# Kernel tuning notes

Measured on AMD Instinct MI355X. Metric: run time of the kernel, lower is better.

## Reference

```python
import jax, jax.numpy as jnp
import numpy as np

B, VD, SD, CD, H, HEADS = 16384, 2048, 1024, 512, 256, 4
DH = H // HEADS
EPS = 1e-5


def layer_norm(x, g, b):
    m = jnp.mean(x, axis=-1, keepdims=True)
    v = jnp.var(x, axis=-1, keepdims=True)
    return (x - m) * jax.lax.rsqrt(v + EPS) * g + b


def setup_inputs() -> dict:
    key = jax.random.key(0)
    ks = jax.random.split(key, 16)
    sc = 0.02
    inp = {
        'fv': jax.random.normal(ks[0], (B, VD), jnp.float32),
        'fs': jax.random.normal(ks[1], (B, SD), jnp.float32),
        'fc': jax.random.normal(ks[2], (B, CD), jnp.float32),
        # projection linears + layernorms
        'Wv': jax.random.normal(ks[3], (H, VD), jnp.float32) * sc,
        'bv': jnp.zeros((H,), jnp.float32),
        'gv': jnp.ones((H,), jnp.float32), 'bev': jnp.zeros((H,), jnp.float32),
        'Ws': jax.random.normal(ks[4], (H, SD), jnp.float32) * sc,
        'bs': jnp.zeros((H,), jnp.float32),
        'gs': jnp.ones((H,), jnp.float32), 'bes': jnp.zeros((H,), jnp.float32),
        'Wc': jax.random.normal(ks[5], (H, CD), jnp.float32) * sc,
        'bc': jnp.zeros((H,), jnp.float32),
        'gc_': jnp.ones((H,), jnp.float32), 'bec': jnp.zeros((H,), jnp.float32),
        # MultiheadAttention packed in-proj and out-proj
        'in_w': jax.random.normal(ks[6], (3 * H, H), jnp.float32) * sc,
        'in_b': jnp.zeros((3 * H,), jnp.float32),
        'out_w': jax.random.normal(ks[7], (H, H), jnp.float32) * sc,
        'out_b': jnp.zeros((H,), jnp.float32),
        # post-attention layernorm
        'gn': jnp.ones((H,), jnp.float32), 'gb': jnp.zeros((H,), jnp.float32),
        # gating MLP: Linear(3H,64) -> GELU -> Linear(64,3) -> softmax
        'g1w': jax.random.normal(ks[8], (64, 3 * H), jnp.float32) * sc,
        'g1b': jnp.zeros((64,), jnp.float32),
        'g2w': jax.random.normal(ks[9], (3, 64), jnp.float32) * sc,
        'g2b': jnp.zeros((3,), jnp.float32),
    }
    return inp


def reference(fv, fs, fc, Wv, bv, gv, bev, Ws, bs, gs, bes, Wc, bc, gc_, bec,
              in_w, in_b, out_w, out_b, gn, gb, g1w, g1b, g2w, g2b):
    v = layer_norm(fv @ Wv.T + bv, gv, bev)   # [B,H]
    s = layer_norm(fs @ Ws.T + bs, gs, bes)
    c = layer_norm(fc @ Wc.T + bc, gc_, bec)
    stack = jnp.stack([v, s, c], axis=1)      # [B,3,H]

    # self-attention over seq=3 (eval mode: dropout off)
    qkv = stack @ in_w.T + in_b               # [B,3,3H]
    q, k, vv = jnp.split(qkv, 3, axis=-1)
    def heads(x):  # [B,3,H] -> [B,HEADS,3,DH]
        return x.reshape(B, 3, HEADS, DH).transpose(0, 2, 1, 3)
    q, k, vv = heads(q), heads(k), heads(vv)
    scores = jnp.einsum('bhqd,bhkd->bhqk', q, k) / jnp.sqrt(jnp.float32(DH))
    attn = jax.nn.softmax(scores, axis=-1)
    ctx = jnp.einsum('bhqk,bhkd->bhqd', attn, vv)
    ctx = ctx.transpose(0, 2, 1, 3).reshape(B, 3, H)
    attended = ctx @ out_w.T + out_b          # [B,3,H]

    attended = layer_norm(attended + stack, gn, gb)
    av, as_, ac = attended[:, 0], attended[:, 1], attended[:, 2]

    h1 = jax.nn.gelu(jnp.concatenate([av, as_, ac], axis=-1) @ g1w.T + g1b, approximate=False)
    gates = jax.nn.softmax(h1 @ g2w.T + g2b, axis=-1)  # [B,3]

    fused = gates[:, 0:1] * av + gates[:, 1:2] * as_ + gates[:, 2:3] * ac
    return (fused, gates)
```

## Files before the change

kernel.cpp:

```cpp
#include <hip/hip_runtime.h>
#include <math.h>


typedef unsigned short u16;
typedef __bf16 bf16x8 __attribute__((ext_vector_type(8)));
typedef float fx4 __attribute__((ext_vector_type(4)));

#define MFMA_BF16(A_, B_, C_) __builtin_amdgcn_mfma_f32_16x16x32_bf16((A_), (B_), (C_), 0, 0, 0)

__device__ __forceinline__ float bf2f(u16 s) {
    union { float f; unsigned u; } c; c.u = ((unsigned)s) << 16; return c.f;
}
__device__ __forceinline__ u16 f2bf(float f) {
    union { float f; unsigned u; } c; c.f = f;
    return (u16)((c.u + 0x7fffu + ((c.u >> 16) & 1u)) >> 16);
}
__device__ __forceinline__ float bfpair_dot(unsigned a, unsigned b) {
    union { unsigned u; float f; } al, ah, bl, bh;
    al.u = a << 16; ah.u = a & 0xffff0000u;
    bl.u = b << 16; bh.u = b & 0xffff0000u;
    return al.f * bl.f + ah.f * bh.f;
}
__device__ __forceinline__ void gld16(void* l, const void* g) {
    __builtin_amdgcn_global_load_lds((const __attribute__((address_space(1))) void*)g,
                                     (__attribute__((address_space(3))) void*)l, 16, 0, 0);
}

__global__ __launch_bounds__(256) void cvt_w(const float* Wv, const float* Ws, const float* Wc,
                                             const float* inw, const float* outw, const float* g1w,
                                             u16* dst) {
    int idx = blockIdx.x * 256 + threadIdx.x;
    const float* src; int rel;
    if      (idx <  524288) { src = Wv;   rel = idx; }
    else if (idx <  786432) { src = Ws;   rel = idx -  524288; }
    else if (idx <  917504) { src = Wc;   rel = idx -  786432; }
    else if (idx < 1114112) { src = inw;  rel = idx -  917504; }
    else if (idx < 1179648) { src = outw; rel = idx - 1114112; }
    else                    { src = g1w;  rel = idx - 1179648; }
    dst[idx] = f2bf(src[rel]);
}

__global__ __launch_bounds__(256, 3) void gemm_ln(
    const float* fv, const float* fs, const float* fc,
    const u16* wWv, const u16* wWs, const u16* wWc,
    const float* bv, const float* gv, const float* bev,
    const float* bs, const float* gs, const float* bes,
    const float* bc, const float* gc_, const float* bec,
    u16* stack) {
    __shared__ alignas(16) char smem[45568];
    u16* sC = (u16*)smem;
    float* redS = (float*)(smem + 43008);
    float* redQ = (float*)(smem + 44032);
    float* mvS  = (float*)(smem + 45056);

    int bid = blockIdx.x;
    int slot, mblk;
    if (bid < 256)      { slot = 0; mblk = bid; }
    else if (bid < 512) { slot = 1; mblk = bid - 256; }
    else                { slot = 2; mblk = bid - 512; }

    const float* A; const u16* W; const float* bias; const float* gg; const float* be; int K;
    if (slot == 0)      { A = fv; W = wWv; bias = bv; gg = gv;  be = bev; K = 2048; }
    else if (slot == 1) { A = fs; W = wWs; bias = bs; gg = gs;  be = bes; K = 1024; }
    else                { A = fc; W = wWc; bias = bc; gg = gc_; be = bec; K = 512;  }

    int t = threadIdx.x, wv = t >> 6, ln = t & 63, q = ln >> 4, l15 = ln & 15;
    int m0 = mblk * 64;

    fx4 zero = {0.f, 0.f, 0.f, 0.f};
    fx4 acc[4][4];
    #pragma unroll
    for (int mi = 0; mi < 4; ++mi)
        #pragma unroll
        for (int ni = 0; ni < 4; ++ni) acc[mi][ni] = zero;

    int rowA = t >> 2, ca = t & 3;
    const float* aBase = A + (size_t)(m0 + rowA) * K + ca * 8;
    int sAwOff = rowA * 40 + ca * 8;

    int bN[4], bKc[4], bDst[4];
    #pragma unroll
    for (int i = 0; i < 4; ++i) {
        int d = wv * 256 + i * 64 + ln;
        bN[i] = d >> 2;
        bKc[i] = (d & 3) ^ ((bN[i] >> 1) & 3);
        bDst[i] = (wv * 256 + i * 64) * 16;
    }

    int niter = K >> 5;

    {
        float4 f0 = *(const float4*)(aBase);
        float4 f1 = *(const float4*)(aBase + 4);
        #pragma unroll
        for (int i = 0; i < 4; ++i)
            gld16(smem + 10240 + bDst[i], W + (size_t)bN[i] * K + bKc[i] * 8);
        union { u16 us[8]; uint4 v; } pk;
        pk.us[0] = f2bf(f0.x); pk.us[1] = f2bf(f0.y); pk.us[2] = f2bf(f0.z); pk.us[3] = f2bf(f0.w);
        pk.us[4] = f2bf(f1.x); pk.us[5] = f2bf(f1.y); pk.us[6] = f2bf(f1.z); pk.us[7] = f2bf(f1.w);
        *(uint4*)((u16*)smem + sAwOff) = pk.v;
    }
    __syncthreads();

    for (int kt = 0; kt < niter; ++kt) {
        int cur = kt & 1, nxt_b = (kt + 1) & 1;
        u16* sAc = (u16*)(smem + cur * 5120);
        u16* sBc = (u16*)(smem + 10240 + cur * 16384);
        int has_next = (kt + 1) < niter;

        float4 nf0, nf1;
        if (has_next) {
            nf0 = *(const float4*)(aBase + (kt + 1) * 32);
            nf1 = *(const float4*)(aBase + (kt + 1) * 32 + 4);
            char* sBn = smem + 10240 + nxt_b * 16384;
            #pragma unroll
            for (int i = 0; i < 4; ++i)
                gld16(sBn + bDst[i], W + (size_t)bN[i] * K + (kt + 1) * 32 + bKc[i] * 8);
        }

        bf16x8 af[4], bfr[4];
        #pragma unroll
        for (int mi = 0; mi < 4; ++mi)
            af[mi] = *(const bf16x8*)(sAc + (mi * 16 + l15) * 40 + q * 8);
        #pragma unroll
        for (int ni = 0; ni < 4; ++ni) {
            int n = wv * 64 + ni * 16 + l15;
            int ch = n * 4 + (q ^ ((n >> 1) & 3));
            bfr[ni] = *(const bf16x8*)(sBc + ch * 8);
        }
        #pragma unroll
        for (int mi = 0; mi < 4; ++mi)
            #pragma unroll
            for (int ni = 0; ni < 4; ++ni)
                acc[mi][ni] = MFMA_BF16(af[mi], bfr[ni], acc[mi][ni]);

        if (has_next) {
            union { u16 us[8]; uint4 v; } pk;
            pk.us[0] = f2bf(nf0.x); pk.us[1] = f2bf(nf0.y); pk.us[2] = f2bf(nf0.z); pk.us[3] = f2bf(nf0.w);
            pk.us[4] = f2bf(nf1.x); pk.us[5] = f2bf(nf1.y); pk.us[6] = f2bf(nf1.z); pk.us[7] = f2bf(nf1.w);
            *(uint4*)((u16*)(smem + nxt_b * 5120) + sAwOff) = pk.v;
        }
        __syncthreads();
    }

    float biasv[4], gvv[4], bevv[4];
    #pragma unroll
    for (int ni = 0; ni < 4; ++ni) {
        int col = wv * 64 + ni * 16 + l15;
        biasv[ni] = bias[col]; gvv[ni] = gg[col]; bevv[ni] = be[col];
    }
    #pragma unroll
    for (int mi = 0; mi < 4; ++mi)
        #pragma unroll
        for (int ni = 0; ni < 4; ++ni)
            #pragma unroll
            for (int r = 0; r < 4; ++r) acc[mi][ni][r] += biasv[ni];
    #pragma unroll
    for (int mi = 0; mi < 4; ++mi) {
        #pragma unroll
        for (int r = 0; r < 4; ++r) {
            float s = 0.f, qq = 0.f;
            #pragma unroll
            for (int ni = 0; ni < 4; ++ni) { float x = acc[mi][ni][r]; s += x; qq += x * x; }
            #pragma unroll
            for (int m = 1; m < 16; m <<= 1) { s += __shfl_xor(s, m, 64); qq += __shfl_xor(qq, m, 64); }
            if (l15 == 0) { int rho = mi * 16 + q * 4 + r; redS[rho * 4 + wv] = s; redQ[rho * 4 + wv] = qq; }
        }
    }
    __syncthreads();
    if (t < 64) {
        float s = redS[t * 4] + redS[t * 4 + 1] + redS[t * 4 + 2] + redS[t * 4 + 3];
        float qq = redQ[t * 4] + redQ[t * 4 + 1] + redQ[t * 4 + 2] + redQ[t * 4 + 3];
        float mean = s * (1.f / 256.f);
        float var = qq * (1.f / 256.f) - mean * mean;
        mvS[t * 2] = mean; mvS[t * 2 + 1] = rsqrtf(var + 1e-5f);
    }
    __syncthreads();
    #pragma unroll
    for (int mi = 0; mi < 4; ++mi) {
        #pragma unroll
        for (int r = 0; r < 4; ++r) {
            int rho = mi * 16 + q * 4 + r;
            float mean = mvS[rho * 2], rstd = mvS[rho * 2 + 1];
            #pragma unroll
            for (int ni = 0; ni < 4; ++ni) {
                int col = wv * 64 + ni * 16 + l15;
                float x = (acc[mi][ni][r] - mean) * rstd * gvv[ni] + bevv[ni];
                sC[rho * 256 + col] = f2bf(x);
            }
        }
    }
    __syncthreads();
    u16* outp = stack + (size_t)m0 * 768 + slot * 256;
    #pragma unroll
    for (int it = 0; it < 8; ++it) {
        int idx = t + it * 256;
        int row = idx >> 5, c = idx & 31;
        uint4 v = *(const uint4*)(sC + row * 256 + c * 8);
        *(uint4*)(outp + (size_t)row * 768 + c * 8) = v;
    }
}

__global__ __launch_bounds__(256) void gemm_qkv(const u16* stack, const u16* W, const float* in_b,
                                                u16* qkv) {
    __shared__ alignas(16) char smem[32768];
    u16* sC = (u16*)smem;

    int t = threadIdx.x, wv = t >> 6, ln = t & 63, q = ln >> 4, l15 = ln & 15;
    int n0 = blockIdx.x * 128, m0 = blockIdx.y * 128;
    int wr = wv >> 1, wc = wv & 1;

    fx4 zero = {0.f, 0.f, 0.f, 0.f};
    fx4 acc[4][4];
    #pragma unroll
    for (int mi = 0; mi < 4; ++mi)
        #pragma unroll
        for (int ni = 0; ni < 4; ++ni) acc[mi][ni] = zero;

    int sR[2], sKc[2], sDst[2];
    #pragma unroll
    for (int i = 0; i < 2; ++i) {
        int d = wv * 128 + i * 64 + ln;
        sR[i] = d >> 2;
        sKc[i] = (d & 3) ^ ((sR[i] >> 1) & 3);
        sDst[i] = (wv * 128 + i * 64) * 16;
    }

    #pragma unroll
    for (int i = 0; i < 2; ++i) {
        gld16(smem + sDst[i],         stack + (size_t)(m0 + sR[i]) * 256 + sKc[i] * 8);
        gld16(smem + 16384 + sDst[i], W     + (size_t)(n0 + sR[i]) * 256 + sKc[i] * 8);
    }
    __syncthreads();

    for (int kt = 0; kt < 8; ++kt) {
        int cur = kt & 1, nxt_b = (kt + 1) & 1;
        if (kt < 7) {
            #pragma unroll
            for (int i = 0; i < 2; ++i) {
                gld16(smem + nxt_b * 8192 + sDst[i],
                      stack + (size_t)(m0 + sR[i]) * 256 + (kt + 1) * 32 + sKc[i] * 8);
                gld16(smem + 16384 + nxt_b * 8192 + sDst[i],
                      W + (size_t)(n0 + sR[i]) * 256 + (kt + 1) * 32 + sKc[i] * 8);
            }
        }
        u16* sAc = (u16*)(smem + cur * 8192);
        u16* sBc = (u16*)(smem + 16384 + cur * 8192);
        bf16x8 af[4], bfr[4];
        #pragma unroll
        for (int mi = 0; mi < 4; ++mi) {
            int r = wr * 64 + mi * 16 + l15;
            int ch = r * 4 + (q ^ ((r >> 1) & 3));
            af[mi] = *(const bf16x8*)(sAc + ch * 8);
        }
        #pragma unroll
        for (int ni = 0; ni < 4; ++ni) {
            int n = wc * 64 + ni * 16 + l15;
            int ch = n * 4 + (q ^ ((n >> 1) & 3));
            bfr[ni] = *(const bf16x8*)(sBc + ch * 8);
        }
        #pragma unroll
        for (int mi = 0; mi < 4; ++mi)
            #pragma unroll
            for (int ni = 0; ni < 4; ++ni)
                acc[mi][ni] = MFMA_BF16(af[mi], bfr[ni], acc[mi][ni]);
        __syncthreads();
    }
    float biasv[4];
    #pragma unroll
    for (int ni = 0; ni < 4; ++ni) biasv[ni] = in_b[n0 + wc * 64 + ni * 16 + l15];
    #pragma unroll
    for (int mi = 0; mi < 4; ++mi)
        #pragma unroll
        for (int ni = 0; ni < 4; ++ni)
            #pragma unroll
            for (int r = 0; r < 4; ++r) {
                int rl = wr * 64 + mi * 16 + q * 4 + r;
                int cl = wc * 64 + ni * 16 + l15;
                sC[rl * 128 + cl] = f2bf(acc[mi][ni][r] + biasv[ni]);
            }
    __syncthreads();
    #pragma unroll
    for (int it = 0; it < 8; ++it) {
        int idx = t + it * 256;
        int row = idx >> 4, c = idx & 15;
        uint4 v = *(const uint4*)(sC + row * 128 + c * 8);
        *(uint4*)(qkv + (size_t)(m0 + row) * 768 + n0 + c * 8) = v;
    }
}

__global__ __launch_bounds__(256) void attn_k(const u16* qkv, u16* ctx) {
    __shared__ alignas(16) char smem[38016];
    u16* qs = (u16*)smem;
    float* sS = (float*)(smem + 36864);

    int t = threadIdx.x, wv = t >> 6, ln = t & 63;
    size_t base = (size_t)blockIdx.x * 8 * 2304;
    #pragma unroll
    for (int i = 0; i < 9; ++i) {
        int d = wv * 576 + i * 64;
        gld16((char*)smem + (size_t)d * 16, qkv + base + (size_t)(d + ln) * 8);
    }
    __syncthreads();
    #pragma unroll
    for (int it = 0; it < 2; ++it) {
        int idx = t + it * 256;
        if (idx < 288) {
            int b = idx / 36, rem = idx % 36, h = rem / 9, pp = rem % 9, i = pp / 3, j = pp % 3;
            const u16* qp = qs + b * 2304 + i * 768 + h * 64;
            const u16* kp = qs + b * 2304 + j * 768 + 256 + h * 64;
            float acc = 0.f;
            #pragma unroll
            for (int c = 0; c < 8; ++c) {
                uint4 qa = *(const uint4*)(qp + c * 8);
                uint4 ka = *(const uint4*)(kp + c * 8);
                acc += bfpair_dot(qa.x, ka.x) + bfpair_dot(qa.y, ka.y) +
                       bfpair_dot(qa.z, ka.z) + bfpair_dot(qa.w, ka.w);
            }
            sS[idx] = acc * 0.125f;
        }
    }
    __syncthreads();
    if (t < 96) {
        int b3 = t * 3;
        float s0 = sS[b3], s1 = sS[b3 + 1], s2 = sS[b3 + 2];
        float m = fmaxf(s0, fmaxf(s1, s2));
        float e0 = __expf(s0 - m), e1 = __expf(s1 - m), e2 = __expf(s2 - m);
        float inv = 1.f / (e0 + e1 + e2);
        sS[b3] = e0 * inv; sS[b3 + 1] = e1 * inv; sS[b3 + 2] = e2 * inv;
    }
    __syncthreads();
    #pragma unroll
    for (int it = 0; it < 3; ++it) {
        int idx = t + it * 256;
        int b = idx / 96, rem = idx % 96, i = rem / 32, c = rem & 31, h = c >> 3;
        int pbase = b * 36 + h * 9 + i * 3;
        float o[8];
        #pragma unroll
        for (int e = 0; e < 8; ++e) o[e] = 0.f;
        #pragma unroll
        for (int j = 0; j < 3; ++j) {
            float p = sS[pbase + j];
            uint4 va = *(const uint4*)(qs + b * 2304 + j * 768 + 512 + c * 8);
            unsigned uu[4] = {va.x, va.y, va.z, va.w};
            #pragma unroll
            for (int pr = 0; pr < 4; ++pr) {
                union { unsigned u; float f; } lo, hi;
                lo.u = uu[pr] << 16; hi.u = uu[pr] & 0xffff0000u;
                o[2 * pr]     += p * lo.f;
                o[2 * pr + 1] += p * hi.f;
            }
        }
        union { u16 us[8]; uint4 v; } pk;
        #pragma unroll
        for (int e = 0; e < 8; ++e) pk.us[e] = f2bf(o[e]);
        *(uint4*)(ctx + (size_t)(blockIdx.x * 8 + b) * 768 + i * 256 + c * 8) = pk.v;
    }
}

__global__ __launch_bounds__(256) void outproj_k(
    const u16* ctx, const u16* W, const float* out_b, const u16* stack,
    const float* gn, const float* gb, const u16* g1w, const float* g1b,
    const float* g2w, const float* g2b, float* outF, float* outG) {
    __shared__ alignas(16) char smem[40960];
    u16* r1 = (u16*)smem;
    u16* sB = (u16*)(smem + 24576);
    float* redS = (float*)(smem + 24576);
    float* redQ = redS + 192;
    float* mvS = redQ + 192;
    float* h1S = (float*)(smem + 26624);
    float* lgS = (float*)(smem + 30720);
    float* gateS = lgS + 48;

    int t = threadIdx.x, wv = t >> 6, ln = t & 63, q = ln >> 4, l15 = ln & 15;
    int gr0 = blockIdx.x * 48, b0 = blockIdx.x * 16;

    #pragma unroll
    for (int i = 0; i < 6; ++i) {
        int d = wv * 384 + i * 64 + ln;
        int row = d >> 5, p = d & 31;
        int kc = p ^ (row & 7);
        gld16((char*)r1 + (wv * 384 + i * 64) * 16, ctx + (size_t)(gr0 + row) * 256 + kc * 8);
    }
    __syncthreads();

    fx4 zero = {0.f, 0.f, 0.f, 0.f};
    fx4 acc[3][4];
    #pragma unroll
    for (int mi = 0; mi < 3; ++mi)
        #pragma unroll
        for (int ni = 0; ni < 4; ++ni) acc[mi][ni] = zero;

    for (int kt = 0; kt < 8; ++kt) {
        #pragma unroll
        for (int i = 0; i < 4; ++i) {
            int d = wv * 256 + i * 64 + ln;
            int n = d >> 2, p = d & 3;
            int kc = p ^ ((n >> 1) & 3);
            gld16((char*)sB + (wv * 256 + i * 64) * 16, W + (size_t)n * 256 + kt * 32 + kc * 8);
        }
        __syncthreads();
        bf16x8 af[3], bfr[4];
        #pragma unroll
        for (int mi = 0; mi < 3; ++mi) {
            int row = mi * 16 + l15;
            int ch = row * 32 + ((kt * 4 + q) ^ (row & 7));
            af[mi] = *(const bf16x8*)(r1 + ch * 8);
        }
        #pragma unroll
        for (int ni = 0; ni < 4; ++ni) {
            int n = wv * 64 + ni * 16 + l15;
            int ch = n * 4 + (q ^ ((n >> 1) & 3));
            bfr[ni] = *(const bf16x8*)(sB + ch * 8);
        }
        #pragma unroll
        for (int mi = 0; mi < 3; ++mi)
            #pragma unroll
            for (int ni = 0; ni < 4; ++ni)
                acc[mi][ni] = MFMA_BF16(af[mi], bfr[ni], acc[mi][ni]);
        __syncthreads();
    }

    #pragma unroll
    for (int i = 0; i < 6; ++i) {
        int d = wv * 384 + i * 64 + ln;
        gld16((char*)r1 + (wv * 384 + i * 64) * 16, stack + (size_t)gr0 * 256 + (size_t)d * 8);
    }
    __syncthreads();

    float obv[4], gnv[4], gbv[4];
    #pragma unroll
    for (int ni = 0; ni < 4; ++ni) {
        int col = wv * 64 + ni * 16 + l15;
        obv[ni] = out_b[col]; gnv[ni] = gn[col]; gbv[ni] = gb[col];
    }
    #pragma unroll
    for (int mi = 0; mi < 3; ++mi)
        #pragma unroll
        for (int ni = 0; ni < 4; ++ni)
            #pragma unroll
            for (int r = 0; r < 4; ++r) {
                int rho = mi * 16 + q * 4 + r;
                int col = wv * 64 + ni * 16 + l15;
                acc[mi][ni][r] += obv[ni] + bf2f(r1[rho * 256 + col]);
            }
    #pragma unroll
    for (int mi = 0; mi < 3; ++mi) {
        #pragma unroll
        for (int r = 0; r < 4; ++r) {
            float s = 0.f, qq = 0.f;
            #pragma unroll
            for (int ni = 0; ni < 4; ++ni) { float x = acc[mi][ni][r]; s += x; qq += x * x; }
            #pragma unroll
            for (int m = 1; m < 16; m <<= 1) { s += __shfl_xor(s, m, 64); qq += __shfl_xor(qq, m, 64); }
            if (l15 == 0) { int rho = mi * 16 + q * 4 + r; redS[rho * 4 + wv] = s; redQ[rho * 4 + wv] = qq; }
        }
    }
    __syncthreads();
    if (t < 48) {
        float s = redS[t * 4] + redS[t * 4 + 1] + redS[t * 4 + 2] + redS[t * 4 + 3];
        float qq = redQ[t * 4] + redQ[t * 4 + 1] + redQ[t * 4 + 2] + redQ[t * 4 + 3];
        float mean = s * (1.f / 256.f);
        float var = qq * (1.f / 256.f) - mean * mean;
        mvS[t * 2] = mean; mvS[t * 2 + 1] = rsqrtf(var + 1e-5f);
    }
    __syncthreads();
    #pragma unroll
    for (int mi = 0; mi < 3; ++mi) {
        #pragma unroll
        for (int r = 0; r < 4; ++r) {
            int rho = mi * 16 + q * 4 + r;
            float mean = mvS[rho * 2], rstd = mvS[rho * 2 + 1];
            int bl = rho / 3, sl = rho - bl * 3;
            #pragma unroll
            for (int ni = 0; ni < 4; ++ni) {
                int col = wv * 64 + ni * 16 + l15;
                float x = (acc[mi][ni][r] - mean) * rstd * gnv[ni] + gbv[ni];
                int k = sl * 256 + col;
                int kidx = k >> 3, wn = k & 7;
                r1[(bl * 96 + (kidx ^ (bl & 7))) * 8 + wn] = f2bf(x);
            }
        }
    }
    __syncthreads();
    fx4 ag = zero;
    for (int kt = 0; kt < 24; ++kt) {
        int bl = l15;
        int kidx = kt * 4 + q;
        bf16x8 afr = *(const bf16x8*)(r1 + (bl * 96 + (kidx ^ (bl & 7))) * 8);
        int n = wv * 16 + l15;
        bf16x8 bfr2 = *(const bf16x8*)(g1w + (size_t)n * 768 + kt * 32 + q * 8);
        ag = MFMA_BF16(afr, bfr2, ag);
    }
    #pragma unroll
    for (int r = 0; r < 4; ++r) {
        int bl = q * 4 + r, n = wv * 16 + l15;
        float x = ag[r] + g1b[n];
        h1S[bl * 64 + n] = 0.5f * x * (1.f + erff(x * 0.70710678118f));
    }
    __syncthreads();
    if (t < 48) {
        int bl = t / 3, s = t - bl * 3;
        float a = g2b[s];
        #pragma unroll
        for (int k = 0; k < 64; ++k) a += h1S[bl * 64 + k] * g2w[s * 64 + k];
        lgS[t] = a;
    }
    __syncthreads();
    if (t < 48) {
        int bl = t / 3, s = t - bl * 3;
        float l0 = lgS[bl * 3], l1 = lgS[bl * 3 + 1], l2 = lgS[bl * 3 + 2];
        float m = fmaxf(l0, fmaxf(l1, l2));
        float e0 = __expf(l0 - m), e1 = __expf(l1 - m), e2 = __expf(l2 - m);
        float inv = 1.f / (e0 + e1 + e2);
        float gsel = ((s == 0) ? e0 : (s == 1) ? e1 : e2) * inv;
        gateS[t] = gsel;
        outG[(size_t)(b0 + bl) * 3 + s] = gsel;
    }
    __syncthreads();
    #pragma unroll
    for (int it = 0; it < 2; ++it) {
        int idx = t + it * 256;
        int b = idx >> 5, c = idx & 31;
        float g0 = gateS[b * 3], g1 = gateS[b * 3 + 1], g2 = gateS[b * 3 + 2];
        float o[8];
        #pragma unroll
        for (int e = 0; e < 8; ++e) o[e] = 0.f;
        #pragma unroll
        for (int s = 0; s < 3; ++s) {
            float gw = (s == 0) ? g0 : (s == 1) ? g1 : g2;
            int kidx = s * 32 + c;
            uint4 raw = *(const uint4*)(r1 + (b * 96 + (kidx ^ (b & 7))) * 8);
            unsigned uu[4] = {raw.x, raw.y, raw.z, raw.w};
            #pragma unroll
            for (int pr = 0; pr < 4; ++pr) {
                union { unsigned u; float f; } lo, hi;
                lo.u = uu[pr] << 16; hi.u = uu[pr] & 0xffff0000u;
                o[2 * pr]     += gw * lo.f;
                o[2 * pr + 1] += gw * hi.f;
            }
        }
        float* op = outF + (size_t)(b0 + b) * 256 + c * 8;
        float4 v0; v0.x = o[0]; v0.y = o[1]; v0.z = o[2]; v0.w = o[3];
        float4 v1; v1.x = o[4]; v1.y = o[5]; v1.z = o[6]; v1.w = o[7];
        *(float4*)op = v0;
        *(float4*)(op + 4) = v1;
    }
}

extern "C" void kernel_launch(void* const* d_in, const int* in_sizes, int n_in,
                              void* d_out, int out_size, void* d_ws, size_t ws_size,
                              hipStream_t stream) {
    (void)in_sizes; (void)n_in; (void)out_size; (void)ws_size;
    const float* fv   = (const float*)d_in[0];
    const float* fs   = (const float*)d_in[1];
    const float* fc   = (const float*)d_in[2];
    const float* Wv   = (const float*)d_in[3];
    const float* bv   = (const float*)d_in[4];
    const float* gv   = (const float*)d_in[5];
    const float* bev  = (const float*)d_in[6];
    const float* Ws   = (const float*)d_in[7];
    const float* bs   = (const float*)d_in[8];
    const float* gs   = (const float*)d_in[9];
    const float* bes  = (const float*)d_in[10];
    const float* Wc   = (const float*)d_in[11];
    const float* bc   = (const float*)d_in[12];
    const float* gc_  = (const float*)d_in[13];
    const float* bec  = (const float*)d_in[14];
    const float* in_w = (const float*)d_in[15];
    const float* in_b = (const float*)d_in[16];
    const float* out_w= (const float*)d_in[17];
    const float* out_b= (const float*)d_in[18];
    const float* gn   = (const float*)d_in[19];
    const float* gb   = (const float*)d_in[20];
    const float* g1w  = (const float*)d_in[21];
    const float* g1b  = (const float*)d_in[22];
    const float* g2w  = (const float*)d_in[23];
    const float* g2b  = (const float*)d_in[24];

    u16* w0    = (u16*)d_ws;
    u16* wWv   = w0;
    u16* wWs   = w0 + 524288;
    u16* wWc   = w0 + 786432;
    u16* wIn   = w0 + 917504;
    u16* wOut  = w0 + 1114112;
    u16* wG1   = w0 + 1179648;
    u16* stack = w0 + 1228800;
    u16* qkv   = w0 + 13811712;
    u16* ctx   = w0 + 51560448;
    float* outF = (float*)d_out;
    float* outG = outF + (size_t)16384 * 256;

    cvt_w<<<4800, 256, 0, stream>>>(Wv, Ws, Wc, in_w, out_w, g1w, w0);
    gemm_ln<<<768, 256, 0, stream>>>(fv, fs, fc, wWv, wWs, wWc,
                                     bv, gv, bev, bs, gs, bes, bc, gc_, bec, stack);
    gemm_qkv<<<dim3(6, 384), 256, 0, stream>>>(stack, wIn, in_b, qkv);
    attn_k<<<2048, 256, 0, stream>>>(qkv, ctx);
    outproj_k<<<1024, 256, 0, stream>>>(ctx, wOut, out_b, stack, gn, gb,
                                        wG1, g1b, g2w, g2b, outF, outG);
}
```

Before: 438.1 us.

## Keep QKV A-tile resident across all N panels and enlarge outproj row tiles

gemm_qkv now loads a 192-row slice of the stacked activations into LDS once. It then loops over the three 256-wide N panels (Q, K, V), streaming only the weight tiles with double buffering, and launches 256 blocks of 512 threads instead of a 6x384 grid. The goal is to stop re-reading the same activation rows once per N tile. The cost is very large LDS use (about 153 KB per block), low occupancy, and a serialized epilogue with extra barriers. outproj_k processes 96 rows (32 batch elements) per block instead of 48, so the out-proj and gate weights are fetched half as often per row, at the cost of more registers, more LDS, and half as many blocks.

```diff
diff --git a/kernel.cpp b/kernel.cpp
--- a/kernel.cpp
+++ b/kernel.cpp
@@ -201,92 +201,106 @@
     }
 }
 
-__global__ __launch_bounds__(256) void gemm_qkv(const u16* stack, const u16* W, const float* in_b,
-                                                u16* qkv) {
-    __shared__ alignas(16) char smem[32768];
-    u16* sC = (u16*)smem;
+__global__ __launch_bounds__(512, 2) void gemm_qkv(const u16* stack, const u16* W, const float* in_b,
+                                                   u16* qkv) {
+    __shared__ alignas(16) char smem[156416];
+    u16* sA = (u16*)smem;
+    u16* sC = (u16*)(smem + 131072);
 
     int t = threadIdx.x, wv = t >> 6, ln = t & 63, q = ln >> 4, l15 = ln & 15;
-    int n0 = blockIdx.x * 128, m0 = blockIdx.y * 128;
     int wr = wv >> 1, wc = wv & 1;
+    int m0 = blockIdx.x * 192;
+
+    #pragma unroll
+    for (int i = 0; i < 12; ++i) {
+        int d = i * 512 + t;
+        int r = d >> 5, p = d & 31;
+        int kc = p ^ (r & 31);
+        gld16((char*)smem + d * 16, stack + (size_t)(m0 + r) * 256 + kc * 8);
+    }
+    int bN[2], bKc[2];
+    #pragma unroll
+    for (int i = 0; i < 2; ++i) {
+        int d = i * 512 + t;
+        bN[i] = d >> 2;
+        bKc[i] = (d & 3) ^ ((bN[i] >> 1) & 3);
+    }
+
+#define QK_STAGE(sstep)                                                              \
+    {                                                                                \
+        int np_ = (sstep) >> 3, kt_ = (sstep) & 7;                                   \
+        char* dst_ = smem + 98304 + ((sstep) & 1) * 16384;                           \
+        _Pragma("unroll")                                                            \
+        for (int i_ = 0; i_ < 2; ++i_)                                               \
+            gld16(dst_ + (i_ * 512 + t) * 16,                                        \
+                  W + (size_t)(np_ * 256 + bN[i_]) * 256 + kt_ * 32 + bKc[i_] * 8);  \
+    }
+
+    QK_STAGE(0);
+    __syncthreads();
 
     fx4 zero = {0.f, 0.f, 0.f, 0.f};
-    fx4 acc[4][4];
-    #pragma unroll
-    for (int mi = 0; mi < 4; ++mi)
-        #pragma unroll
-        for (int ni = 0; ni < 4; ++ni) acc[mi][ni] = zero;
-
-    int sR[2], sKc[2], sDst[2];
-    #pragma unroll
-    for (int i = 0; i < 2; ++i) {
-        int d = wv * 128 + i * 64 + ln;
-        sR[i] = d >> 2;
-        sKc[i] = (d & 3) ^ ((sR[i] >> 1) & 3);
-        sDst[i] = (wv * 128 + i * 64) * 16;
-    }
-
-    #pragma unroll
-    for (int i = 0; i < 2; ++i) {
-        gld16(smem + sDst[i],         stack + (size_t)(m0 + sR[i]) * 256 + sKc[i] * 8);
-        gld16(smem + 16384 + sDst[i], W     + (size_t)(n0 + sR[i]) * 256 + sKc[i] * 8);
-    }
-    __syncthreads();
-
-    for (int kt = 0; kt < 8; ++kt) {
-        int cur = kt & 1, nxt_b = (kt + 1) & 1;
-        if (kt < 7) {
-            #pragma unroll
-            for (int i = 0; i < 2; ++i) {
-                gld16(smem + nxt_b * 8192 + sDst[i],
-                      stack + (size_t)(m0 + sR[i]) * 256 + (kt + 1) * 32 + sKc[i] * 8);
-                gld16(smem + 16384 + nxt_b * 8192 + sDst[i],
-                      W + (size_t)(n0 + sR[i]) * 256 + (kt + 1) * 32 + sKc[i] * 8);
-            }
-        }
-        u16* sAc = (u16*)(smem + cur * 8192);
-        u16* sBc = (u16*)(smem + 16384 + cur * 8192);
-        bf16x8 af[4], bfr[4];
-        #pragma unroll
-        for (int mi = 0; mi < 4; ++mi) {
-            int r = wr * 64 + mi * 16 + l15;
-            int ch = r * 4 + (q ^ ((r >> 1) & 3));
-            af[mi] = *(const bf16x8*)(sAc + ch * 8);
-        }
-        #pragma unroll
-        for (int ni = 0; ni < 4; ++ni) {
-            int n = wc * 64 + ni * 16 + l15;
-            int ch = n * 4 + (q ^ ((n >> 1) & 3));
-            bfr[ni] = *(const bf16x8*)(sBc + ch * 8);
-        }
-        #pragma unroll
-        for (int mi = 0; mi < 4; ++mi)
-            #pragma unroll
-            for (int ni = 0; ni < 4; ++ni)
-                acc[mi][ni] = MFMA_BF16(af[mi], bfr[ni], acc[mi][ni]);
-        __syncthreads();
-    }
-    float biasv[4];
-    #pragma unroll
-    for (int ni = 0; ni < 4; ++ni) biasv[ni] = in_b[n0 + wc * 64 + ni * 16 + l15];
-    #pragma unroll
-    for (int mi = 0; mi < 4; ++mi)
-        #pragma unroll
-        for (int ni = 0; ni < 4; ++ni)
-            #pragma unroll
-            for (int r = 0; r < 4; ++r) {
-                int rl = wr * 64 + mi * 16 + q * 4 + r;
-                int cl = wc * 64 + ni * 16 + l15;
-                sC[rl * 128 + cl] = f2bf(acc[mi][ni][r] + biasv[ni]);
-            }
-    __syncthreads();
-    #pragma unroll
-    for (int it = 0; it < 8; ++it) {
-        int idx = t + it * 256;
-        int row = idx >> 4, c = idx & 15;
-        uint4 v = *(const uint4*)(sC + row * 128 + c * 8);
-        *(uint4*)(qkv + (size_t)(m0 + row) * 768 + n0 + c * 8) = v;
-    }
+    for (int np = 0; np < 3; ++np) {
+        fx4 acc[3][8];
+        #pragma unroll
+        for (int mi = 0; mi < 3; ++mi)
+            #pragma unroll
+            for (int ni = 0; ni < 8; ++ni) acc[mi][ni] = zero;
+
+        for (int kt = 0; kt < 8; ++kt) {
+            int s = np * 8 + kt;
+            if (s + 1 < 24) QK_STAGE(s + 1);
+            const u16* sBc = (const u16*)(smem + 98304 + (s & 1) * 16384);
+            bf16x8 af[3], bfr[8];
+            #pragma unroll
+            for (int mi = 0; mi < 3; ++mi) {
+                int row = wr * 48 + mi * 16 + l15;
+                int ck = kt * 4 + q;
+                af[mi] = *(const bf16x8*)(sA + (row * 32 + (ck ^ (row & 31))) * 8);
+            }
+            #pragma unroll
+            for (int ni = 0; ni < 8; ++ni) {
+                int n = wc * 128 + ni * 16 + l15;
+                int ch = n * 4 + (q ^ ((n >> 1) & 3));
+                bfr[ni] = *(const bf16x8*)(sBc + ch * 8);
+            }
+            #pragma unroll
+            for (int mi = 0; mi < 3; ++mi)
+                #pragma unroll
+                for (int ni = 0; ni < 8; ++ni)
+                    acc[mi][ni] = MFMA_BF16(af[mi], bfr[ni], acc[mi][ni]);
+            __syncthreads();
+        }
+
+        float biasv[8];
+        #pragma unroll
+        for (int ni = 0; ni < 8; ++ni) biasv[ni] = in_b[np * 256 + wc * 128 + ni * 16 + l15];
+        #pragma unroll
+        for (int g = 0; g < 4; ++g) {
+            if (wr == g) {
+                #pragma unroll
+                for (int mi = 0; mi < 3; ++mi)
+                    #pragma unroll
+                    for (int ni = 0; ni < 8; ++ni)
+                        #pragma unroll
+                        for (int r = 0; r < 4; ++r) {
+                            int lr = mi * 16 + q * 4 + r;
+                            int cl = wc * 128 + ni * 16 + l15;
+                            sC[lr * 264 + cl] = f2bf(acc[mi][ni][r] + biasv[ni]);
+                        }
+            }
+            __syncthreads();
+            #pragma unroll
+            for (int i = 0; i < 3; ++i) {
+                int idx = i * 512 + t;
+                int row = idx >> 5, c = idx & 31;
+                uint4 v = *(const uint4*)(sC + row * 264 + c * 8);
+                *(uint4*)(qkv + (size_t)(m0 + g * 48 + row) * 768 + np * 256 + c * 8) = v;
+            }
+            __syncthreads();
+        }
+    }
+#undef QK_STAGE
 }
 
 __global__ __launch_bounds__(256) void attn_k(const u16* qkv, u16* ctx) {
@@ -362,47 +376,47 @@
     const u16* ctx, const u16* W, const float* out_b, const u16* stack,
     const float* gn, const float* gb, const u16* g1w, const float* g1b,
     const float* g2w, const float* g2b, float* outF, float* outG) {
-    __shared__ alignas(16) char smem[40960];
+    __shared__ alignas(16) char smem[65536];
     u16* r1 = (u16*)smem;
-    u16* sB = (u16*)(smem + 24576);
-    float* redS = (float*)(smem + 24576);
-    float* redQ = redS + 192;
-    float* mvS = redQ + 192;
-    float* h1S = (float*)(smem + 26624);
-    float* lgS = (float*)(smem + 30720);
-    float* gateS = lgS + 48;
+    u16* sB = (u16*)(smem + 49152);
+    float* redS = (float*)(smem + 49152);
+    float* redQ = (float*)(smem + 50688);
+    float* mvS  = (float*)(smem + 52224);
+    float* h1S  = (float*)(smem + 53248);
+    float* lgS  = (float*)(smem + 61440);
+    float* gateS= (float*)(smem + 61824);
 
     int t = threadIdx.x, wv = t >> 6, ln = t & 63, q = ln >> 4, l15 = ln & 15;
-    int gr0 = blockIdx.x * 48, b0 = blockIdx.x * 16;
-
-    #pragma unroll
-    for (int i = 0; i < 6; ++i) {
-        int d = wv * 384 + i * 64 + ln;
+    int gr0 = blockIdx.x * 96, b0 = blockIdx.x * 32;
+
+    #pragma unroll
+    for (int i = 0; i < 12; ++i) {
+        int d = i * 256 + t;
         int row = d >> 5, p = d & 31;
         int kc = p ^ (row & 7);
-        gld16((char*)r1 + (wv * 384 + i * 64) * 16, ctx + (size_t)(gr0 + row) * 256 + kc * 8);
+        gld16((char*)r1 + d * 16, ctx + (size_t)(gr0 + row) * 256 + kc * 8);
     }
     __syncthreads();
 
     fx4 zero = {0.f, 0.f, 0.f, 0.f};
-    fx4 acc[3][4];
-    #pragma unroll
-    for (int mi = 0; mi < 3; ++mi)
+    fx4 acc[6][4];
+    #pragma unroll
+    for (int mi = 0; mi < 6; ++mi)
         #pragma unroll
         for (int ni = 0; ni < 4; ++ni) acc[mi][ni] = zero;
 
     for (int kt = 0; kt < 8; ++kt) {
         #pragma unroll
         for (int i = 0; i < 4; ++i) {
-            int d = wv * 256 + i * 64 + ln;
+            int d = i * 256 + t;
             int n = d >> 2, p = d & 3;
             int kc = p ^ ((n >> 1) & 3);
-            gld16((char*)sB + (wv * 256 + i * 64) * 16, W + (size_t)n * 256 + kt * 32 + kc * 8);
+            gld16((char*)sB + d * 16, W + (size_t)n * 256 + kt * 32 + kc * 8);
         }
         __syncthreads();
-        bf16x8 af[3], bfr[4];
-        #pragma unroll
-        for (int mi = 0; mi < 3; ++mi) {
+        bf16x8 af[6], bfr[4];
+        #pragma unroll
+        for (int mi = 0; mi < 6; ++mi) {
             int row = mi * 16 + l15;
             int ch = row * 32 + ((kt * 4 + q) ^ (row & 7));
             af[mi] = *(const bf16x8*)(r1 + ch * 8);
@@ -414,7 +428,7 @@
             bfr[ni] = *(const bf16x8*)(sB + ch * 8);
         }
         #pragma unroll
-        for (int mi = 0; mi < 3; ++mi)
+        for (int mi = 0; mi < 6; ++mi)
             #pragma unroll
             for (int ni = 0; ni < 4; ++ni)
                 acc[mi][ni] = MFMA_BF16(af[mi], bfr[ni], acc[mi][ni]);
@@ -422,9 +436,9 @@
     }
 
     #pragma unroll
-    for (int i = 0; i < 6; ++i) {
-        int d = wv * 384 + i * 64 + ln;
-        gld16((char*)r1 + (wv * 384 + i * 64) * 16, stack + (size_t)gr0 * 256 + (size_t)d * 8);
+    for (int i = 0; i < 12; ++i) {
+        int d = i * 256 + t;
+        gld16((char*)r1 + d * 16, stack + (size_t)gr0 * 256 + (size_t)d * 8);
     }
     __syncthreads();
 
@@ -435,7 +449,7 @@
         obv[ni] = out_b[col]; gnv[ni] = gn[col]; gbv[ni] = gb[col];
     }
     #pragma unroll
-    for (int mi = 0; mi < 3; ++mi)
+    for (int mi = 0; mi < 6; ++mi)
         #pragma unroll
         for (int ni = 0; ni < 4; ++ni)
             #pragma unroll
@@ -445,7 +459,7 @@
                 acc[mi][ni][r] += obv[ni] + bf2f(r1[rho * 256 + col]);
             }
     #pragma unroll
-    for (int mi = 0; mi < 3; ++mi) {
+    for (int mi = 0; mi < 6; ++mi) {
         #pragma unroll
         for (int r = 0; r < 4; ++r) {
             float s = 0.f, qq = 0.f;
@@ -457,7 +471,7 @@
         }
     }
     __syncthreads();
-    if (t < 48) {
+    if (t < 96) {
         float s = redS[t * 4] + redS[t * 4 + 1] + redS[t * 4 + 2] + redS[t * 4 + 3];
         float qq = redQ[t * 4] + redQ[t * 4 + 1] + redQ[t * 4 + 2] + redQ[t * 4 + 3];
         float mean = s * (1.f / 256.f);
@@ -466,7 +480,7 @@
     }
     __syncthreads();
     #pragma unroll
-    for (int mi = 0; mi < 3; ++mi) {
+    for (int mi = 0; mi < 6; ++mi) {
         #pragma unroll
         for (int r = 0; r < 4; ++r) {
             int rho = mi * 16 + q * 4 + r;
@@ -483,23 +497,26 @@
         }
     }
     __syncthreads();
-    fx4 ag = zero;
+    fx4 ag0 = zero, ag1 = zero;
     for (int kt = 0; kt < 24; ++kt) {
-        int bl = l15;
         int kidx = kt * 4 + q;
-        bf16x8 afr = *(const bf16x8*)(r1 + (bl * 96 + (kidx ^ (bl & 7))) * 8);
         int n = wv * 16 + l15;
         bf16x8 bfr2 = *(const bf16x8*)(g1w + (size_t)n * 768 + kt * 32 + q * 8);
-        ag = MFMA_BF16(afr, bfr2, ag);
+        bf16x8 a0 = *(const bf16x8*)(r1 + (l15 * 96 + (kidx ^ (l15 & 7))) * 8);
+        bf16x8 a1 = *(const bf16x8*)(r1 + ((16 + l15) * 96 + (kidx ^ (l15 & 7))) * 8);
+        ag0 = MFMA_BF16(a0, bfr2, ag0);
+        ag1 = MFMA_BF16(a1, bfr2, ag1);
     }
     #pragma unroll
     for (int r = 0; r < 4; ++r) {
         int bl = q * 4 + r, n = wv * 16 + l15;
-        float x = ag[r] + g1b[n];
-        h1S[bl * 64 + n] = 0.5f * x * (1.f + erff(x * 0.70710678118f));
-    }
-    __syncthreads();
-    if (t < 48) {
+        float x0 = ag0[r] + g1b[n];
+        float x1 = ag1[r] + g1b[n];
+        h1S[bl * 64 + n]        = 0.5f * x0 * (1.f + erff(x0 * 0.70710678118f));
+        h1S[(16 + bl) * 64 + n] = 0.5f * x1 * (1.f + erff(x1 * 0.70710678118f));
+    }
+    __syncthreads();
+    if (t < 96) {
         int bl = t / 3, s = t - bl * 3;
         float a = g2b[s];
         #pragma unroll
@@ -507,7 +524,7 @@
         lgS[t] = a;
     }
     __syncthreads();
-    if (t < 48) {
+    if (t < 96) {
         int bl = t / 3, s = t - bl * 3;
         float l0 = lgS[bl * 3], l1 = lgS[bl * 3 + 1], l2 = lgS[bl * 3 + 2];
         float m = fmaxf(l0, fmaxf(l1, l2));
@@ -519,7 +536,7 @@
     }
     __syncthreads();
     #pragma unroll
-    for (int it = 0; it < 2; ++it) {
+    for (int it = 0; it < 4; ++it) {
         int idx = t + it * 256;
         int b = idx >> 5, c = idx & 31;
         float g0 = gateS[b * 3], g1 = gateS[b * 3 + 1], g2 = gateS[b * 3 + 2];
@@ -594,8 +611,8 @@
     cvt_w<<<4800, 256, 0, stream>>>(Wv, Ws, Wc, in_w, out_w, g1w, w0);
     gemm_ln<<<768, 256, 0, stream>>>(fv, fs, fc, wWv, wWs, wWc,
                                      bv, gv, bev, bs, gs, bes, bc, gc_, bec, stack);
-    gemm_qkv<<<dim3(6, 384), 256, 0, stream>>>(stack, wIn, in_b, qkv);
+    gemm_qkv<<<256, 512, 0, stream>>>(stack, wIn, in_b, qkv);
     attn_k<<<2048, 256, 0, stream>>>(qkv, ctx);
-    outproj_k<<<1024, 256, 0, stream>>>(ctx, wOut, out_b, stack, gn, gb,
-                                        wG1, g1b, g2w, g2b, outF, outG);
-}
+    outproj_k<<<512, 256, 0, stream>>>(ctx, wOut, out_b, stack, gn, gb,
+                                       wG1, g1b, g2w, g2b, outF, outG);
+}
```

Result: slower. 453.9 us (+3.6%).

## Pre-convert fv/fs to bf16 and triple-buffer QKV GEMM loads

Applied to the files above, without the earlier changes.

Adds a kernel that converts the fv and fs activations to bf16 in scratch space reused from the qkv buffer. gemm_ln can then stream A tiles into LDS with async global_load_lds and a swizzled layout, instead of loading fp32 through registers and converting inside the K loop. The QKV GEMM moves from double to triple buffering with manual vmcnt waits, a single barrier per iteration and raised priority around the MFMAs. The trade-off is an extra full pass writing and rereading about 96MB of bf16 activations, in exchange for a lighter inner loop.

```diff
diff --git a/kernel.cpp b/kernel.cpp
--- a/kernel.cpp
+++ b/kernel.cpp
@@ -7,6 +7,7 @@
 typedef float fx4 __attribute__((ext_vector_type(4)));
 
 #define MFMA_BF16(A_, B_, C_) __builtin_amdgcn_mfma_f32_16x16x32_bf16((A_), (B_), (C_), 0, 0, 0)
+#define WAIT_VM(N) asm volatile("s_waitcnt vmcnt(" #N ")" ::: "memory")
 
 __device__ __forceinline__ float bf2f(u16 s) {
     union { float f; unsigned u; } c; c.u = ((unsigned)s) << 16; return c.f;
@@ -40,8 +41,21 @@
     dst[idx] = f2bf(src[rel]);
 }
 
+__global__ __launch_bounds__(256) void cvt_a(const float* fv, const float* fs, u16* dst) {
+    size_t idx8 = ((size_t)blockIdx.x * 256 + threadIdx.x) * 8;
+    const float* src; size_t rel;
+    if (idx8 < 33554432) { src = fv; rel = idx8; }
+    else                 { src = fs; rel = idx8 - 33554432; }
+    float4 a = *(const float4*)(src + rel);
+    float4 b = *(const float4*)(src + rel + 4);
+    union { u16 us[8]; uint4 v; } pk;
+    pk.us[0] = f2bf(a.x); pk.us[1] = f2bf(a.y); pk.us[2] = f2bf(a.z); pk.us[3] = f2bf(a.w);
+    pk.us[4] = f2bf(b.x); pk.us[5] = f2bf(b.y); pk.us[6] = f2bf(b.z); pk.us[7] = f2bf(b.w);
+    *(uint4*)(dst + idx8) = pk.v;
+}
+
 __global__ __launch_bounds__(256, 3) void gemm_ln(
-    const float* fv, const float* fs, const float* fc,
+    const float* fcIn, const u16* Av, const u16* As,
     const u16* wWv, const u16* wWs, const u16* wWc,
     const float* bv, const float* gv, const float* bev,
     const float* bs, const float* gs, const float* bes,
@@ -59,10 +73,11 @@
     else if (bid < 512) { slot = 1; mblk = bid - 256; }
     else                { slot = 2; mblk = bid - 512; }
 
-    const float* A; const u16* W; const float* bias; const float* gg; const float* be; int K;
-    if (slot == 0)      { A = fv; W = wWv; bias = bv; gg = gv;  be = bev; K = 2048; }
-    else if (slot == 1) { A = fs; W = wWs; bias = bs; gg = gs;  be = bes; K = 1024; }
-    else                { A = fc; W = wWc; bias = bc; gg = gc_; be = bec; K = 512;  }
+    const u16* Ab; const float* Af; const u16* W;
+    const float* bias; const float* gg; const float* be; int K;
+    if (slot == 0)      { Ab = Av; Af = 0;    W = wWv; bias = bv; gg = gv;  be = bev; K = 2048; }
+    else if (slot == 1) { Ab = As; Af = 0;    W = wWs; bias = bs; gg = gs;  be = bes; K = 1024; }
+    else                { Ab = 0;  Af = fcIn; W = wWc; bias = bc; gg = gc_; be = bec; K = 512;  }
 
     int t = threadIdx.x, wv = t >> 6, ln = t & 63, q = ln >> 4, l15 = ln & 15;
     int m0 = mblk * 64;
@@ -74,9 +89,10 @@
         #pragma unroll
         for (int ni = 0; ni < 4; ++ni) acc[mi][ni] = zero;
 
-    int rowA = t >> 2, ca = t & 3;
-    const float* aBase = A + (size_t)(m0 + rowA) * K + ca * 8;
-    int sAwOff = rowA * 40 + ca * 8;
+    int aR = t >> 2, aP = t & 3;
+    int aKc = aP ^ ((aR >> 1) & 3);
+    const float* aBase = (slot == 2) ? (Af + (size_t)(m0 + aR) * 512 + aP * 8) : (const float*)0;
+    int sAwOff = aR * 40 + aP * 8;
 
     int bN[4], bKc[4], bDst[4];
     #pragma unroll
@@ -89,7 +105,12 @@
 
     int niter = K >> 5;
 
-    {
+    if (slot < 2) {
+        gld16(smem + t * 16, Ab + (size_t)(m0 + aR) * K + aKc * 8);
+        #pragma unroll
+        for (int i = 0; i < 4; ++i)
+            gld16(smem + 10240 + bDst[i], W + (size_t)bN[i] * K + bKc[i] * 8);
+    } else {
         float4 f0 = *(const float4*)(aBase);
         float4 f1 = *(const float4*)(aBase + 4);
         #pragma unroll
@@ -102,6 +123,7 @@
     }
     __syncthreads();
 
+    int aSw = (l15 >> 1) & 3;
     for (int kt = 0; kt < niter; ++kt) {
         int cur = kt & 1, nxt_b = (kt + 1) & 1;
         u16* sAc = (u16*)(smem + cur * 5120);
@@ -110,8 +132,13 @@
 
         float4 nf0, nf1;
         if (has_next) {
-            nf0 = *(const float4*)(aBase + (kt + 1) * 32);
-            nf1 = *(const float4*)(aBase + (kt + 1) * 32 + 4);
+            if (slot < 2) {
+                gld16(smem + nxt_b * 5120 + t * 16,
+                      Ab + (size_t)(m0 + aR) * K + (kt + 1) * 32 + aKc * 8);
+            } else {
+                nf0 = *(const float4*)(aBase + (kt + 1) * 32);
+                nf1 = *(const float4*)(aBase + (kt + 1) * 32 + 4);
+            }
             char* sBn = smem + 10240 + nxt_b * 16384;
             #pragma unroll
             for (int i = 0; i < 4; ++i)
@@ -119,9 +146,17 @@
         }
 
         bf16x8 af[4], bfr[4];
-        #pragma unroll
-        for (int mi = 0; mi < 4; ++mi)
-            af[mi] = *(const bf16x8*)(sAc + (mi * 16 + l15) * 40 + q * 8);
+        if (slot < 2) {
+            #pragma unroll
+            for (int mi = 0; mi < 4; ++mi) {
+                int r = mi * 16 + l15;
+                af[mi] = *(const bf16x8*)(sAc + (r * 4 + (q ^ aSw)) * 8);
+            }
+        } else {
+            #pragma unroll
+            for (int mi = 0; mi < 4; ++mi)
+                af[mi] = *(const bf16x8*)(sAc + (mi * 16 + l15) * 40 + q * 8);
+        }
         #pragma unroll
         for (int ni = 0; ni < 4; ++ni) {
             int n = wv * 64 + ni * 16 + l15;
@@ -134,7 +169,7 @@
             for (int ni = 0; ni < 4; ++ni)
                 acc[mi][ni] = MFMA_BF16(af[mi], bfr[ni], acc[mi][ni]);
 
-        if (has_next) {
+        if (has_next && slot == 2) {
             union { u16 us[8]; uint4 v; } pk;
             pk.us[0] = f2bf(nf0.x); pk.us[1] = f2bf(nf0.y); pk.us[2] = f2bf(nf0.z); pk.us[3] = f2bf(nf0.w);
             pk.us[4] = f2bf(nf1.x); pk.us[5] = f2bf(nf1.y); pk.us[6] = f2bf(nf1.z); pk.us[7] = f2bf(nf1.w);
@@ -201,9 +236,9 @@
     }
 }
 
-__global__ __launch_bounds__(256) void gemm_qkv(const u16* stack, const u16* W, const float* in_b,
-                                                u16* qkv) {
-    __shared__ alignas(16) char smem[32768];
+__global__ __launch_bounds__(256, 3) void gemm_qkv(const u16* stack, const u16* W, const float* in_b,
+                                                   u16* qkv) {
+    __shared__ alignas(16) char smem[49152];
     u16* sC = (u16*)smem;
 
     int t = threadIdx.x, wv = t >> 6, ln = t & 63, q = ln >> 4, l15 = ln & 15;
@@ -217,35 +252,40 @@
         #pragma unroll
         for (int ni = 0; ni < 4; ++ni) acc[mi][ni] = zero;
 
-    int sR[2], sKc[2], sDst[2];
+    int sR[2], sKc[2];
     #pragma unroll
     for (int i = 0; i < 2; ++i) {
         int d = wv * 128 + i * 64 + ln;
         sR[i] = d >> 2;
         sKc[i] = (d & 3) ^ ((sR[i] >> 1) & 3);
-        sDst[i] = (wv * 128 + i * 64) * 16;
-    }
-
-    #pragma unroll
-    for (int i = 0; i < 2; ++i) {
-        gld16(smem + sDst[i],         stack + (size_t)(m0 + sR[i]) * 256 + sKc[i] * 8);
-        gld16(smem + 16384 + sDst[i], W     + (size_t)(n0 + sR[i]) * 256 + sKc[i] * 8);
-    }
-    __syncthreads();
-
+    }
+
+#define QK_ISSUE(ktile, bufoff)                                                         \
+    {                                                                                   \
+        char* bA_ = smem + (bufoff);                                                    \
+        char* bB_ = bA_ + 8192;                                                         \
+        _Pragma("unroll")                                                               \
+        for (int i_ = 0; i_ < 2; ++i_) {                                                \
+            gld16(bA_ + (wv * 128 + i_ * 64) * 16,                                      \
+                  stack + (size_t)(m0 + sR[i_]) * 256 + (ktile) * 32 + sKc[i_] * 8);    \
+            gld16(bB_ + (wv * 128 + i_ * 64) * 16,                                      \
+                  W + (size_t)(n0 + sR[i_]) * 256 + (ktile) * 32 + sKc[i_] * 8);        \
+        }                                                                               \
+    }
+
+    QK_ISSUE(0, 0);
+    QK_ISSUE(1, 16384);
+    int cb = 0;
     for (int kt = 0; kt < 8; ++kt) {
-        int cur = kt & 1, nxt_b = (kt + 1) & 1;
-        if (kt < 7) {
-            #pragma unroll
-            for (int i = 0; i < 2; ++i) {
-                gld16(smem + nxt_b * 8192 + sDst[i],
-                      stack + (size_t)(m0 + sR[i]) * 256 + (kt + 1) * 32 + sKc[i] * 8);
-                gld16(smem + 16384 + nxt_b * 8192 + sDst[i],
-                      W + (size_t)(n0 + sR[i]) * 256 + (kt + 1) * 32 + sKc[i] * 8);
-            }
-        }
-        u16* sAc = (u16*)(smem + cur * 8192);
-        u16* sBc = (u16*)(smem + 16384 + cur * 8192);
+        if (kt < 7) { WAIT_VM(4); } else { WAIT_VM(0); }
+        __builtin_amdgcn_sched_barrier(0);
+        __builtin_amdgcn_s_barrier();
+        __builtin_amdgcn_sched_barrier(0);
+        int nb = cb + 2; if (nb >= 3) nb -= 3;
+        if (kt + 2 < 8) QK_ISSUE(kt + 2, nb * 16384);
+
+        const u16* sAc = (const u16*)(smem + cb * 16384);
+        const u16* sBc = (const u16*)(smem + cb * 16384 + 8192);
         bf16x8 af[4], bfr[4];
         #pragma unroll
         for (int mi = 0; mi < 4; ++mi) {
@@ -259,13 +299,18 @@
             int ch = n * 4 + (q ^ ((n >> 1) & 3));
             bfr[ni] = *(const bf16x8*)(sBc + ch * 8);
         }
+        __builtin_amdgcn_s_setprio(1);
         #pragma unroll
         for (int mi = 0; mi < 4; ++mi)
             #pragma unroll
             for (int ni = 0; ni < 4; ++ni)
                 acc[mi][ni] = MFMA_BF16(af[mi], bfr[ni], acc[mi][ni]);
-        __syncthreads();
-    }
+        __builtin_amdgcn_s_setprio(0);
+        cb += 1; if (cb >= 3) cb -= 3;
+    }
+#undef QK_ISSUE
+    __syncthreads();
+
     float biasv[4];
     #pragma unroll
     for (int ni = 0; ni < 4; ++ni) biasv[ni] = in_b[n0 + wc * 64 + ni * 16 + l15];
@@ -588,11 +633,15 @@
     u16* stack = w0 + 1228800;
     u16* qkv   = w0 + 13811712;
     u16* ctx   = w0 + 51560448;
+    u16* Abf  = qkv;
+    u16* Av   = Abf;
+    u16* Asb  = Abf + 33554432;
     float* outF = (float*)d_out;
     float* outG = outF + (size_t)16384 * 256;
 
     cvt_w<<<4800, 256, 0, stream>>>(Wv, Ws, Wc, in_w, out_w, g1w, w0);
-    gemm_ln<<<768, 256, 0, stream>>>(fv, fs, fc, wWv, wWs, wWc,
+    cvt_a<<<24576, 256, 0, stream>>>(fv, fs, Abf);
+    gemm_ln<<<768, 256, 0, stream>>>(fc, Av, Asb, wWv, wWs, wWc,
                                      bv, gv, bev, bs, gs, bes, bc, gc_, bec, stack);
     gemm_qkv<<<dim3(6, 384), 256, 0, stream>>>(stack, wIn, in_b, qkv);
     attn_k<<<2048, 256, 0, stream>>>(qkv, ctx);
```

New measurement: 479.9 us. +9.5%, slower.
